# Optimization experiments

Measured on AMD Instinct MI355X. Metric: run time of the kernel, lower is better.

## Reference

```python
import jax, jax.numpy as jnp
import numpy as np

P_DROP = 0.5

def _dropout(x, key):
    keep = jax.random.bernoulli(key, 1.0 - P_DROP, x.shape)
    return jnp.where(keep, x / (1.0 - P_DROP), 0.0)

def _sage_mean_agg(src, dst, feat_src, h_self, n_dst, key):
    # SAGEMeanAgg: dropout both inputs, copy_src gather, segment mean, add, relu
    k1, k2 = jax.random.split(key)
    feat_src = _dropout(feat_src, k1)
    h_self = _dropout(h_self, k2)
    msg = feat_src[src]                                   # [E, d] gather
    summ = jax.ops.segment_sum(msg, dst, num_segments=n_dst)
    deg = jax.ops.segment_sum(jnp.ones((dst.shape[0],), msg.dtype), dst, num_segments=n_dst)
    neigh = jnp.where(deg[:, None] > 0, summ / jnp.maximum(deg, 1.0)[:, None], 0.0)
    return jax.nn.relu(neigh + h_self)

def setup_inputs() -> dict:
    key = jax.random.key(0)
    ks = jax.random.split(key, 12)
    N_total, d_in, d_hid, d_out = 1200000, 128, 256, 47
    N0, N1, N2 = 10000, 100000, 1000000
    E0, E1 = 100000, 1000000
    return {
        "features": jax.random.normal(ks[0], (N_total, d_in), jnp.float32),
        "s0": jax.random.randint(ks[1], (N0,), 0, N_total),
        "s1": jax.random.randint(ks[2], (N1,), 0, N_total),
        "s2": jax.random.randint(ks[3], (N2,), 0, N_total),
        "src0": jax.random.randint(ks[4], (E0,), 0, N1),
        "dst0": jax.random.randint(ks[5], (E0,), 0, N0),
        "src1": jax.random.randint(ks[6], (E1,), 0, N2),
        "dst1": jax.random.randint(ks[7], (E1,), 0, N1),
        "W1": jax.random.normal(ks[8], (d_in, d_hid), jnp.float32) * 0.05,
        "b1": jnp.zeros((d_hid,), jnp.float32),
        "W2": jax.random.normal(ks[9], (d_hid, d_out), jnp.float32) * 0.05,
        "b2": jnp.zeros((d_out,), jnp.float32),
    }

def reference(features, s0, s1, s2, src0, dst0, src1, dst1, W1, b1, W2, b2):
    N0, N1 = s0.shape[0], s1.shape[0]
    dk = jax.random.split(jax.random.key(42), 3)
    h0 = features[s0]
    h1 = features[s1]
    h2 = features[s2]
    # layer 0 over 2 hops (shared linear W1)
    a0 = _sage_mean_agg(src0, dst0, h1, h0, N0, dk[0])
    n0 = a0 @ W1 + b1
    a1 = _sage_mean_agg(src1, dst1, h2, h1, N1, dk[1])
    n1 = a1 @ W1 + b1
    # layer 1 over 1 hop
    a = _sage_mean_agg(src0, dst0, n1, n0, N0, dk[2])
    return a @ W2 + b2
```

## Files before the change

kernel.cpp:

```cpp
#include <hip/hip_runtime.h>
#include <hip/hip_bf16.h>

__host__ __device__ __forceinline__ unsigned rotl32(unsigned x, int d) {
  return (x << d) | (x >> (32 - d));
}

__host__ __device__ __forceinline__ void threefry2x32(
    unsigned k0, unsigned k1, unsigned x0, unsigned x1,
    unsigned& o0, unsigned& o1) {
  unsigned ks2 = k0 ^ k1 ^ 0x1BD11BDAu;
  unsigned v0 = x0 + k0, v1 = x1 + k1;
#define TF_R(r) { v0 += v1; v1 = rotl32(v1, (r)); v1 ^= v0; }
  TF_R(13) TF_R(15) TF_R(26) TF_R(6)  v0 += k1;  v1 += ks2 + 1u;
  TF_R(17) TF_R(29) TF_R(16) TF_R(24) v0 += ks2; v1 += k0 + 2u;
  TF_R(13) TF_R(15) TF_R(26) TF_R(6)  v0 += k0;  v1 += k1 + 3u;
  TF_R(17) TF_R(29) TF_R(16) TF_R(24) v0 += k1;  v1 += ks2 + 4u;
  TF_R(13) TF_R(15) TF_R(26) TF_R(6)  v0 += ks2; v1 += k0 + 5u;
#undef TF_R
  o0 = v0; o1 = v1;
}

__device__ __forceinline__ float drop_scale(unsigned ka, unsigned kb,
                                            unsigned pos) {
  unsigned o0, o1;
  threefry2x32(ka, kb, 0u, pos, o0, o1);
  return ((o0 ^ o1) >> 31) ? 0.0f : 2.0f;
}

__device__ __forceinline__ float bf2f(unsigned short u) {
  unsigned x = ((unsigned)u) << 16;
  float f;
  __builtin_memcpy(&f, &x, 4);
  return f;
}
__device__ __forceinline__ unsigned short f2bf(float f) {
  __hip_bfloat16 h = __float2bfloat16(f);
  unsigned short u;
  __builtin_memcpy(&u, &h, 2);
  return u;
}

__global__ __launch_bounds__(256) void k_count(const int* __restrict__ dst,
                                               int* __restrict__ deg, int E) {
  int e = blockIdx.x * 256 + threadIdx.x;
  if (e < E) atomicAdd(&deg[dst[e]], 1);
}

__global__ __launch_bounds__(256) void k_scan1(const int* __restrict__ d,
                                               int* __restrict__ o,
                                               int* __restrict__ bsum, int n) {
  __shared__ int ls[256];
  int t = threadIdx.x;
  int base = blockIdx.x * 1024 + t * 4;
  int v[4], s = 0;
#pragma unroll
  for (int q = 0; q < 4; ++q) {
    int i = base + q;
    v[q] = (i < n) ? d[i] : 0;
    s += v[q];
  }
  ls[t] = s;
  __syncthreads();
  for (int off = 1; off < 256; off <<= 1) {
    int x = (t >= off) ? ls[t - off] : 0;
    __syncthreads();
    ls[t] += x;
    __syncthreads();
  }
  int run = ls[t] - s;
  if (t == 255) bsum[blockIdx.x] = ls[255];
#pragma unroll
  for (int q = 0; q < 4; ++q) {
    int i = base + q;
    if (i < n) o[i] = run;
    run += v[q];
  }
}

__global__ __launch_bounds__(256) void k_scan3(int* __restrict__ o,
                                               const int* __restrict__ bx,
                                               int n) {
  int t = threadIdx.x;
  int add = bx[blockIdx.x];
  int base = blockIdx.x * 1024 + t * 4;
#pragma unroll
  for (int q = 0; q < 4; ++q) {
    int i = base + q;
    if (i < n) o[i] += add;
  }
}

__global__ __launch_bounds__(256) void k_fill(
    const int* __restrict__ src, const int* __restrict__ dst,
    const int* __restrict__ sel, const int* __restrict__ off,
    int* __restrict__ cur, int* __restrict__ csr_r, int* __restrict__ csr_g,
    int E) {
  int e = blockIdx.x * 256 + threadIdx.x;
  if (e >= E) return;
  int d = dst[e];
  int pos = off[d] + atomicAdd(&cur[d], 1);
  int r = src[e];
  csr_r[pos] = r;
  csr_g[pos] = sel[r];
}

__global__ __launch_bounds__(256) void k_agg128(
    const float* __restrict__ feats, const int* __restrict__ off,
    const int* __restrict__ csr_r, const int* __restrict__ csr_g,
    const int* __restrict__ sel_self, unsigned short* __restrict__ outbf,
    int N, unsigned kfa, unsigned kfb, unsigned kha, unsigned khb) {
  int wave = (blockIdx.x * 256 + threadIdx.x) >> 6;
  int lane = threadIdx.x & 63;
  if (wave >= N) return;
  int beg = off[wave], end = off[wave + 1];
  float acc0 = 0.f, acc1 = 0.f;
  for (int base = beg; base < end; base += 64) {
    int idx = base + lane;
    int r_l = 0, g_l = 0;
    if (idx < end) { r_l = csr_r[idx]; g_l = csr_g[idx]; }
    int cnt = min(64, end - base);
    for (int b = 0; b < cnt; ++b) {
      int r = __shfl(r_l, b), g = __shfl(g_l, b);
      float2 f = *(const float2*)(feats + (size_t)g * 128 + lane * 2);
      unsigned p = (unsigned)r * 128u + (unsigned)(lane * 2);
      acc0 += f.x * drop_scale(kfa, kfb, p);
      acc1 += f.y * drop_scale(kfa, kfb, p + 1);
    }
  }
  float deg = (float)(end - beg);
  float inv = deg > 0.f ? 1.0f / deg : 0.f;
  float n0 = acc0 * inv, n1 = acc1 * inv;
  float2 sf = *(const float2*)(feats + (size_t)sel_self[wave] * 128 + lane * 2);
  unsigned ps = (unsigned)wave * 128u + (unsigned)(lane * 2);
  float v0 = n0 + sf.x * drop_scale(kha, khb, ps);
  float v1 = n1 + sf.y * drop_scale(kha, khb, ps + 1);
  v0 = v0 > 0.f ? v0 : 0.f;
  v1 = v1 > 0.f ? v1 : 0.f;
  ushort2 u;
  u.x = f2bf(v0);
  u.y = f2bf(v1);
  *(ushort2*)(outbf + (size_t)wave * 128 + lane * 2) = u;
}

__global__ __launch_bounds__(256) void k_agg256(
    const unsigned short* __restrict__ X, const int* __restrict__ off,
    const int* __restrict__ csr_r, const unsigned short* __restrict__ self,
    unsigned short* __restrict__ outbf, int N,
    unsigned kfa, unsigned kfb, unsigned kha, unsigned khb) {
  int wave = (blockIdx.x * 256 + threadIdx.x) >> 6;
  int lane = threadIdx.x & 63;
  if (wave >= N) return;
  int beg = off[wave], end = off[wave + 1];
  float acc[4] = {0.f, 0.f, 0.f, 0.f};
  for (int base = beg; base < end; base += 64) {
    int idx = base + lane;
    int r_l = 0;
    if (idx < end) r_l = csr_r[idx];
    int cnt = min(64, end - base);
    for (int b = 0; b < cnt; ++b) {
      int r = __shfl(r_l, b);
      ushort4 raw = ((const ushort4*)(X + (size_t)r * 256))[lane];
      unsigned p = (unsigned)r * 256u + (unsigned)(lane * 4);
      acc[0] += bf2f(raw.x) * drop_scale(kfa, kfb, p);
      acc[1] += bf2f(raw.y) * drop_scale(kfa, kfb, p + 1);
      acc[2] += bf2f(raw.z) * drop_scale(kfa, kfb, p + 2);
      acc[3] += bf2f(raw.w) * drop_scale(kfa, kfb, p + 3);
    }
  }
  float deg = (float)(end - beg);
  float inv = deg > 0.f ? 1.0f / deg : 0.f;
  ushort4 sr = ((const ushort4*)(self + (size_t)wave * 256))[lane];
  unsigned ps = (unsigned)wave * 256u + (unsigned)(lane * 4);
  float sv[4] = {bf2f(sr.x), bf2f(sr.y), bf2f(sr.z), bf2f(sr.w)};
  ushort4 u;
  unsigned short* up = (unsigned short*)&u;
#pragma unroll
  for (int c = 0; c < 4; ++c) {
    float v = acc[c] * inv + sv[c] * drop_scale(kha, khb, ps + c);
    up[c] = f2bf(v > 0.f ? v : 0.f);
  }
  ((ushort4*)(outbf + (size_t)wave * 256))[lane] = u;
}

__global__ __launch_bounds__(256) void k_prepW(const float* __restrict__ W1,
                                               unsigned short* __restrict__ W1T) {
  int tid = blockIdx.x * 256 + threadIdx.x;
  int n = tid >> 7, k = tid & 127;
  W1T[n * 128 + k] = f2bf(W1[k * 256 + n]);
}

typedef short v8s __attribute__((ext_vector_type(8)));
typedef float v4f __attribute__((ext_vector_type(4)));

__global__ __launch_bounds__(256) void k_gemm1(
    const unsigned short* __restrict__ A, const unsigned short* __restrict__ W1T,
    const float* __restrict__ bias, unsigned short* __restrict__ C, int M) {
  __shared__ unsigned short As[128 * 72];
  __shared__ unsigned short Bs[128 * 72];
  const int t = threadIdx.x;
  const int r0 = blockIdx.x * 128, n0 = blockIdx.y * 128;
  const int wv = t >> 6, lane = t & 63;
  const int mb = (wv >> 1) * 64, nb = (wv & 1) * 64;
  const int qm = lane & 15, quad = lane >> 4;
  v4f acc[4][4];
#pragma unroll
  for (int i = 0; i < 4; ++i)
#pragma unroll
    for (int j = 0; j < 4; ++j) acc[i][j] = (v4f){0.f, 0.f, 0.f, 0.f};

  for (int kt = 0; kt < 128; kt += 64) {
#pragma unroll
    for (int it = 0; it < 4; ++it) {
      int i = t + it * 256;
      int r = i >> 3, c = i & 7;
      uint4 v = make_uint4(0, 0, 0, 0);
      int gr = r0 + r;
      if (gr < M) v = ((const uint4*)A)[(size_t)gr * 16 + (kt >> 3) + c];
      *(uint4*)&As[r * 72 + c * 8] = v;
    }
#pragma unroll
    for (int it = 0; it < 4; ++it) {
      int i = t + it * 256;
      int n = i >> 3, c = i & 7;
      uint4 v = ((const uint4*)W1T)[(size_t)(n0 + n) * 16 + (kt >> 3) + c];
      *(uint4*)&Bs[n * 72 + c * 8] = v;
    }
    __syncthreads();
#pragma unroll
    for (int kk = 0; kk < 64; kk += 32) {
      v8s af[4], bf_[4];
#pragma unroll
      for (int i = 0; i < 4; ++i)
        af[i] = *(const v8s*)&As[(mb + i * 16 + qm) * 72 + kk + quad * 8];
#pragma unroll
      for (int j = 0; j < 4; ++j)
        bf_[j] = *(const v8s*)&Bs[(nb + j * 16 + qm) * 72 + kk + quad * 8];
#pragma unroll
      for (int i = 0; i < 4; ++i)
#pragma unroll
        for (int j = 0; j < 4; ++j)
          acc[i][j] = __builtin_amdgcn_mfma_f32_16x16x32_bf16(
              af[i], bf_[j], acc[i][j], 0, 0, 0);
    }
    __syncthreads();
  }
  const int col_base = n0 + nb + qm;
  float bj[4];
#pragma unroll
  for (int j = 0; j < 4; ++j) bj[j] = bias[col_base + j * 16];
#pragma unroll
  for (int i = 0; i < 4; ++i) {
    int row = r0 + mb + i * 16 + quad * 4;
#pragma unroll
    for (int reg = 0; reg < 4; ++reg) {
      int rr = row + reg;
      if (rr < M) {
#pragma unroll
        for (int j = 0; j < 4; ++j)
          C[(size_t)rr * 256 + col_base + j * 16] = f2bf(acc[i][j][reg] + bj[j]);
      }
    }
  }
}

__global__ __launch_bounds__(256) void k_gemm2(
    const unsigned short* __restrict__ A, const float* __restrict__ W2,
    const float* __restrict__ b2, float* __restrict__ out, int M) {
  __shared__ float Ws[256 * 47];
  __shared__ unsigned short As[32 * 264];
  const int t = threadIdx.x;
  for (int i = t; i < 256 * 47; i += 256) Ws[i] = W2[i];
  const int r0 = blockIdx.x * 32;
#pragma unroll
  for (int it = 0; it < 4; ++it) {
    int i = t + it * 256;
    int r = i >> 5, c = i & 31;
    uint4 v = make_uint4(0, 0, 0, 0);
    if (r0 + r < M) v = ((const uint4*)A)[(size_t)(r0 + r) * 32 + c];
    *(uint4*)&As[r * 264 + c * 8] = v;
  }
  __syncthreads();
  for (int o = t; o < 32 * 47; o += 256) {
    int r = o / 47, n = o - r * 47;
    if (r0 + r >= M) continue;
    float acc = b2[n];
#pragma unroll 8
    for (int k = 0; k < 256; ++k)
      acc = fmaf(bf2f(As[r * 264 + k]), Ws[k * 47 + n], acc);
    out[(size_t)(r0 + r) * 47 + n] = acc;
  }
}

static inline size_t alignup(size_t x) { return (x + 255) & ~(size_t)255; }

extern "C" void kernel_launch(void* const* d_in, const int* in_sizes, int n_in,
                              void* d_out, int out_size, void* d_ws,
                              size_t ws_size, hipStream_t stream) {
  const float* features = (const float*)d_in[0];
  const int* s0   = (const int*)d_in[1];
  const int* s1   = (const int*)d_in[2];
  const int* s2   = (const int*)d_in[3];
  const int* src0 = (const int*)d_in[4];
  const int* dst0 = (const int*)d_in[5];
  const int* src1 = (const int*)d_in[6];
  const int* dst1 = (const int*)d_in[7];
  const float* W1 = (const float*)d_in[8];
  const float* b1 = (const float*)d_in[9];
  const float* W2 = (const float*)d_in[10];
  const float* b2 = (const float*)d_in[11];
  float* out = (float*)d_out;

  const int N0 = in_sizes[1], N1 = in_sizes[2];
  const int E0 = in_sizes[4], E1 = in_sizes[6];

  unsigned dk[3][2], kfs[3][2], khs[3][2];
  for (int i = 0; i < 3; ++i)
    threefry2x32(0u, 42u, 0u, (unsigned)i, dk[i][0], dk[i][1]);
  for (int i = 0; i < 3; ++i) {
    threefry2x32(dk[i][0], dk[i][1], 0u, 0u, kfs[i][0], kfs[i][1]);
    threefry2x32(dk[i][0], dk[i][1], 0u, 1u, khs[i][0], khs[i][1]);
  }

  char* p = (char*)d_ws;
  auto take = [&](size_t bytes) {
    char* r = p;
    p += alignup(bytes);
    return r;
  };
  unsigned short* a1bf = (unsigned short*)take((size_t)N1 * 128 * 2);
  unsigned short* n1bf = (unsigned short*)take((size_t)N1 * 256 * 2);
  unsigned short* a0bf = (unsigned short*)take((size_t)N0 * 128 * 2);
  unsigned short* n0bf = (unsigned short*)take((size_t)N0 * 256 * 2);
  unsigned short* a2bf = (unsigned short*)take((size_t)N0 * 256 * 2);
  unsigned short* w1t  = (unsigned short*)take(256 * 128 * 2);
  int* off1  = (int*)take((size_t)(N1 + 2) * 4);
  int* deg1  = (int*)take((size_t)(N1 + 2) * 4);
  int* cur1  = (int*)take((size_t)N1 * 4);
  int* off0  = (int*)take((size_t)(N0 + 2) * 4);
  int* deg0  = (int*)take((size_t)(N0 + 2) * 4);
  int* cur0  = (int*)take((size_t)N0 * 4);
  int* bsum  = (int*)take(1024 * 4);
  int* bsumx = (int*)take(1024 * 4);
  int* dummy = (int*)take(1024 * 4);
  int* csr1_r = (int*)take((size_t)E1 * 4);
  int* csr1_g = (int*)take((size_t)E1 * 4);
  int* csr0_r = (int*)take((size_t)E0 * 4);
  int* csr0_g = (int*)take((size_t)E0 * 4);

  hipMemsetAsync(deg1, 0, (size_t)(N1 + 2) * 4, stream);
  hipMemsetAsync(deg0, 0, (size_t)(N0 + 2) * 4, stream);
  hipMemsetAsync(cur1, 0, (size_t)N1 * 4, stream);
  hipMemsetAsync(cur0, 0, (size_t)N0 * 4, stream);

  k_prepW<<<128, 256, 0, stream>>>(W1, w1t);
  k_count<<<(E1 + 255) / 256, 256, 0, stream>>>(dst1, deg1, E1);
  k_count<<<(E0 + 255) / 256, 256, 0, stream>>>(dst0, deg0, E0);

  {
    int n = N1 + 1, B = (n + 1023) / 1024;
    k_scan1<<<B, 256, 0, stream>>>(deg1, off1, bsum, n);
    k_scan1<<<1, 256, 0, stream>>>(bsum, bsumx, dummy, B);
    k_scan3<<<B, 256, 0, stream>>>(off1, bsumx, n);
  }
  {
    int n = N0 + 1, B = (n + 1023) / 1024;
    k_scan1<<<B, 256, 0, stream>>>(deg0, off0, bsum, n);
    k_scan1<<<1, 256, 0, stream>>>(bsum, bsumx, dummy, B);
    k_scan3<<<B, 256, 0, stream>>>(off0, bsumx, n);
  }

  k_fill<<<(E1 + 255) / 256, 256, 0, stream>>>(src1, dst1, s2, off1, cur1,
                                               csr1_r, csr1_g, E1);
  k_fill<<<(E0 + 255) / 256, 256, 0, stream>>>(src0, dst0, s1, off0, cur0,
                                               csr0_r, csr0_g, E0);

  k_agg128<<<(N1 + 3) / 4, 256, 0, stream>>>(
      features, off1, csr1_r, csr1_g, s1, a1bf, N1,
      kfs[1][0], kfs[1][1], khs[1][0], khs[1][1]);
  {
    dim3 g((N1 + 127) / 128, 2);
    k_gemm1<<<g, 256, 0, stream>>>(a1bf, w1t, b1, n1bf, N1);
  }

  k_agg128<<<(N0 + 3) / 4, 256, 0, stream>>>(
      features, off0, csr0_r, csr0_g, s0, a0bf, N0,
      kfs[0][0], kfs[0][1], khs[0][0], khs[0][1]);
  {
    dim3 g((N0 + 127) / 128, 2);
    k_gemm1<<<g, 256, 0, stream>>>(a0bf, w1t, b1, n0bf, N0);
  }

  k_agg256<<<(N0 + 3) / 4, 256, 0, stream>>>(
      n1bf, off0, csr0_r, n0bf, a2bf, N0,
      kfs[2][0], kfs[2][1], khs[2][0], khs[2][1]);
  k_gemm2<<<(N0 + 31) / 32, 256, 0, stream>>>(a2bf, W2, b2, out, N0);
}
```

Before: 1.250 ms.

## Merge per-hop kernels into combined launches and move the second GEMM to MFMA

Graph-build, aggregation and first-GEMM kernels for both hops are merged into single launches over concatenated index ranges, which cuts the launch count. The memsets are replaced with a zero kernel. The two CSR arrays are packed into int2 and a write-offset copy replaces the separate cursor array. The 128-wide gather loop is unrolled by two. The output GEMM now uses bf16 MFMA with a hi/lo split of W2 to keep near-fp32 accuracy, in place of scalar LDS FMA; the split doubles the MFMA count.

```diff
diff --git a/kernel.cpp b/kernel.cpp
--- a/kernel.cpp
+++ b/kernel.cpp
@@ -1,5 +1,8 @@
 #include <hip/hip_runtime.h>
 #include <hip/hip_bf16.h>
+
+typedef short v8s __attribute__((ext_vector_type(8)));
+typedef float v4f __attribute__((ext_vector_type(4)));
 
 __host__ __device__ __forceinline__ unsigned rotl32(unsigned x, int d) {
   return (x << d) | (x >> (32 - d));
@@ -40,18 +43,58 @@
   return u;
 }
 
-__global__ __launch_bounds__(256) void k_count(const int* __restrict__ dst,
-                                               int* __restrict__ deg, int E) {
+__global__ __launch_bounds__(256) void k_zero(int* __restrict__ a, int na,
+                                              int* __restrict__ b, int nb) {
+  int i = blockIdx.x * 256 + threadIdx.x;
+  if (i < na) a[i] = 0;
+  if (i < nb) b[i] = 0;
+}
+
+__global__ __launch_bounds__(256) void k_prep(
+    const float* __restrict__ W1, unsigned short* __restrict__ W1T,
+    const float* __restrict__ W2, unsigned short* __restrict__ W2Th,
+    unsigned short* __restrict__ W2Tl) {
+  int tid = blockIdx.x * 256 + threadIdx.x;
+  if (tid < 32768) {
+    int n = tid >> 7, k = tid & 127;
+    W1T[n * 128 + k] = f2bf(W1[k * 256 + n]);
+  } else if (tid < 32768 + 48 * 256) {
+    int i = tid - 32768;
+    int n = i >> 8, k = i & 255;
+    float w = (n < 47) ? W2[k * 47 + n] : 0.f;
+    unsigned short hi = f2bf(w);
+    float r = w - bf2f(hi);
+    W2Th[n * 256 + k] = hi;
+    W2Tl[n * 256 + k] = f2bf(r);
+  }
+}
+
+__global__ __launch_bounds__(256) void k_countm(
+    const int* __restrict__ dst1, int* __restrict__ deg1, int E1,
+    const int* __restrict__ dst0, int* __restrict__ deg0, int E0) {
   int e = blockIdx.x * 256 + threadIdx.x;
-  if (e < E) atomicAdd(&deg[dst[e]], 1);
-}
-
-__global__ __launch_bounds__(256) void k_scan1(const int* __restrict__ d,
-                                               int* __restrict__ o,
-                                               int* __restrict__ bsum, int n) {
+  if (e < E1) {
+    atomicAdd(&deg1[dst1[e]], 1);
+  } else {
+    int e0 = e - E1;
+    if (e0 < E0) atomicAdd(&deg0[dst0[e0]], 1);
+  }
+}
+
+__global__ __launch_bounds__(256) void k_scan1m(
+    const int* __restrict__ d1, int* __restrict__ o1, int* __restrict__ b1,
+    int n1, int B1,
+    const int* __restrict__ d0, int* __restrict__ o0, int* __restrict__ b0,
+    int n0) {
   __shared__ int ls[256];
+  const int* d; int* o; int* bs; int n; int blk;
+  if ((int)blockIdx.x < B1) {
+    d = d1; o = o1; bs = b1; n = n1; blk = blockIdx.x;
+  } else {
+    d = d0; o = o0; bs = b0; n = n0; blk = blockIdx.x - B1;
+  }
   int t = threadIdx.x;
-  int base = blockIdx.x * 1024 + t * 4;
+  int base = blk * 1024 + t * 4;
   int v[4], s = 0;
 #pragma unroll
   for (int q = 0; q < 4; ++q) {
@@ -68,7 +111,7 @@
     __syncthreads();
   }
   int run = ls[t] - s;
-  if (t == 255) bsum[blockIdx.x] = ls[255];
+  if (t == 255) bs[blk] = ls[255];
 #pragma unroll
   for (int q = 0; q < 4; ++q) {
     int i = base + q;
@@ -77,49 +120,136 @@
   }
 }
 
-__global__ __launch_bounds__(256) void k_scan3(int* __restrict__ o,
-                                               const int* __restrict__ bx,
-                                               int n) {
+__device__ __forceinline__ void scan_chunk(const int* __restrict__ d,
+                                           int* __restrict__ o, int n,
+                                           int* ls) {
   int t = threadIdx.x;
-  int add = bx[blockIdx.x];
-  int base = blockIdx.x * 1024 + t * 4;
+  int base = t * 4;
+  int v[4], s = 0;
 #pragma unroll
   for (int q = 0; q < 4; ++q) {
     int i = base + q;
-    if (i < n) o[i] += add;
-  }
-}
-
-__global__ __launch_bounds__(256) void k_fill(
-    const int* __restrict__ src, const int* __restrict__ dst,
-    const int* __restrict__ sel, const int* __restrict__ off,
-    int* __restrict__ cur, int* __restrict__ csr_r, int* __restrict__ csr_g,
-    int E) {
+    v[q] = (i < n) ? d[i] : 0;
+    s += v[q];
+  }
+  ls[t] = s;
+  __syncthreads();
+  for (int off = 1; off < 256; off <<= 1) {
+    int x = (t >= off) ? ls[t - off] : 0;
+    __syncthreads();
+    ls[t] += x;
+    __syncthreads();
+  }
+  int run = ls[t] - s;
+#pragma unroll
+  for (int q = 0; q < 4; ++q) {
+    int i = base + q;
+    if (i < n) o[i] = run;
+    run += v[q];
+  }
+}
+
+__global__ __launch_bounds__(256) void k_scanmid(
+    const int* __restrict__ b1, int* __restrict__ x1, int B1,
+    const int* __restrict__ b0, int* __restrict__ x0, int B0) {
+  __shared__ int ls[256];
+  scan_chunk(b1, x1, B1, ls);
+  __syncthreads();
+  scan_chunk(b0, x0, B0, ls);
+}
+
+__global__ __launch_bounds__(256) void k_scan3m(
+    int* __restrict__ o1, int* __restrict__ w1, const int* __restrict__ x1,
+    int n1, int B1,
+    int* __restrict__ o0, int* __restrict__ w0, const int* __restrict__ x0,
+    int n0) {
+  int* o; int* w; const int* xx; int n; int blk;
+  if ((int)blockIdx.x < B1) {
+    o = o1; w = w1; xx = x1; n = n1; blk = blockIdx.x;
+  } else {
+    o = o0; w = w0; xx = x0; n = n0; blk = blockIdx.x - B1;
+  }
+  int t = threadIdx.x;
+  int add = xx[blk];
+  int base = blk * 1024 + t * 4;
+#pragma unroll
+  for (int q = 0; q < 4; ++q) {
+    int i = base + q;
+    if (i < n) {
+      int v = o[i] + add;
+      o[i] = v;
+      if (i < n - 1) w[i] = v;
+    }
+  }
+}
+
+__global__ __launch_bounds__(256) void k_fillm(
+    const int* __restrict__ src1, const int* __restrict__ dst1,
+    const int* __restrict__ s2, int* __restrict__ woff1,
+    int2* __restrict__ csr1, int E1,
+    const int* __restrict__ src0, const int* __restrict__ dst0,
+    const int* __restrict__ s1, int* __restrict__ woff0,
+    int2* __restrict__ csr0, int E0) {
   int e = blockIdx.x * 256 + threadIdx.x;
-  if (e >= E) return;
-  int d = dst[e];
-  int pos = off[d] + atomicAdd(&cur[d], 1);
-  int r = src[e];
-  csr_r[pos] = r;
-  csr_g[pos] = sel[r];
-}
-
-__global__ __launch_bounds__(256) void k_agg128(
-    const float* __restrict__ feats, const int* __restrict__ off,
-    const int* __restrict__ csr_r, const int* __restrict__ csr_g,
-    const int* __restrict__ sel_self, unsigned short* __restrict__ outbf,
-    int N, unsigned kfa, unsigned kfb, unsigned kha, unsigned khb) {
+  if (e < E1) {
+    int d = dst1[e];
+    int pos = atomicAdd(&woff1[d], 1);
+    int r = src1[e];
+    csr1[pos] = make_int2(r, s2[r]);
+  } else {
+    int e0 = e - E1;
+    if (e0 < E0) {
+      int d = dst0[e0];
+      int pos = atomicAdd(&woff0[d], 1);
+      int r = src0[e0];
+      csr0[pos] = make_int2(r, s1[r]);
+    }
+  }
+}
+
+__global__ __launch_bounds__(256) void k_agg128m(
+    const float* __restrict__ feats,
+    const int* __restrict__ off1, const int2* __restrict__ csr1,
+    const int* __restrict__ sel1,
+    const int* __restrict__ off0, const int2* __restrict__ csr0,
+    const int* __restrict__ sel0,
+    unsigned short* __restrict__ outbf, int N1, int Ntot,
+    unsigned k1fa, unsigned k1fb, unsigned k1ha, unsigned k1hb,
+    unsigned k0fa, unsigned k0fb, unsigned k0ha, unsigned k0hb) {
   int wave = (blockIdx.x * 256 + threadIdx.x) >> 6;
   int lane = threadIdx.x & 63;
-  if (wave >= N) return;
-  int beg = off[wave], end = off[wave + 1];
+  if (wave >= Ntot) return;
+  const int* off; const int2* csr; const int* sel;
+  unsigned kfa, kfb, kha, khb; int w;
+  if (wave < N1) {
+    off = off1; csr = csr1; sel = sel1;
+    kfa = k1fa; kfb = k1fb; kha = k1ha; khb = k1hb; w = wave;
+  } else {
+    off = off0; csr = csr0; sel = sel0;
+    kfa = k0fa; kfb = k0fb; kha = k0ha; khb = k0hb; w = wave - N1;
+  }
+  int beg = off[w], end = off[w + 1];
   float acc0 = 0.f, acc1 = 0.f;
   for (int base = beg; base < end; base += 64) {
     int idx = base + lane;
-    int r_l = 0, g_l = 0;
-    if (idx < end) { r_l = csr_r[idx]; g_l = csr_g[idx]; }
+    int2 rg = make_int2(0, 0);
+    if (idx < end) rg = csr[idx];
+    int r_l = rg.x, g_l = rg.y;
     int cnt = min(64, end - base);
-    for (int b = 0; b < cnt; ++b) {
+    int b = 0;
+    for (; b + 2 <= cnt; b += 2) {
+      int ra = __shfl(r_l, b),     ga = __shfl(g_l, b);
+      int rb = __shfl(r_l, b + 1), gb = __shfl(g_l, b + 1);
+      float2 fa = *(const float2*)(feats + (size_t)ga * 128 + lane * 2);
+      float2 fb = *(const float2*)(feats + (size_t)gb * 128 + lane * 2);
+      unsigned pa = (unsigned)ra * 128u + (unsigned)(lane * 2);
+      unsigned pb = (unsigned)rb * 128u + (unsigned)(lane * 2);
+      acc0 += fa.x * drop_scale(kfa, kfb, pa);
+      acc1 += fa.y * drop_scale(kfa, kfb, pa + 1);
+      acc0 += fb.x * drop_scale(kfa, kfb, pb);
+      acc1 += fb.y * drop_scale(kfa, kfb, pb + 1);
+    }
+    if (b < cnt) {
       int r = __shfl(r_l, b), g = __shfl(g_l, b);
       float2 f = *(const float2*)(feats + (size_t)g * 128 + lane * 2);
       unsigned p = (unsigned)r * 128u + (unsigned)(lane * 2);
@@ -130,8 +260,8 @@
   float deg = (float)(end - beg);
   float inv = deg > 0.f ? 1.0f / deg : 0.f;
   float n0 = acc0 * inv, n1 = acc1 * inv;
-  float2 sf = *(const float2*)(feats + (size_t)sel_self[wave] * 128 + lane * 2);
-  unsigned ps = (unsigned)wave * 128u + (unsigned)(lane * 2);
+  float2 sf = *(const float2*)(feats + (size_t)sel[w] * 128 + lane * 2);
+  unsigned ps = (unsigned)w * 128u + (unsigned)(lane * 2);
   float v0 = n0 + sf.x * drop_scale(kha, khb, ps);
   float v1 = n1 + sf.y * drop_scale(kha, khb, ps + 1);
   v0 = v0 > 0.f ? v0 : 0.f;
@@ -144,7 +274,7 @@
 
 __global__ __launch_bounds__(256) void k_agg256(
     const unsigned short* __restrict__ X, const int* __restrict__ off,
-    const int* __restrict__ csr_r, const unsigned short* __restrict__ self,
+    const int2* __restrict__ csr, const unsigned short* __restrict__ self,
     unsigned short* __restrict__ outbf, int N,
     unsigned kfa, unsigned kfb, unsigned kha, unsigned khb) {
   int wave = (blockIdx.x * 256 + threadIdx.x) >> 6;
@@ -155,7 +285,7 @@
   for (int base = beg; base < end; base += 64) {
     int idx = base + lane;
     int r_l = 0;
-    if (idx < end) r_l = csr_r[idx];
+    if (idx < end) r_l = csr[idx].x;
     int cnt = min(64, end - base);
     for (int b = 0; b < cnt; ++b) {
       int r = __shfl(r_l, b);
@@ -181,16 +311,6 @@
   }
   ((ushort4*)(outbf + (size_t)wave * 256))[lane] = u;
 }
-
-__global__ __launch_bounds__(256) void k_prepW(const float* __restrict__ W1,
-                                               unsigned short* __restrict__ W1T) {
-  int tid = blockIdx.x * 256 + threadIdx.x;
-  int n = tid >> 7, k = tid & 127;
-  W1T[n * 128 + k] = f2bf(W1[k * 256 + n]);
-}
-
-typedef short v8s __attribute__((ext_vector_type(8)));
-typedef float v4f __attribute__((ext_vector_type(4)));
 
 __global__ __launch_bounds__(256) void k_gemm1(
     const unsigned short* __restrict__ A, const unsigned short* __restrict__ W1T,
@@ -264,30 +384,40 @@
 }
 
 __global__ __launch_bounds__(256) void k_gemm2(
-    const unsigned short* __restrict__ A, const float* __restrict__ W2,
-    const float* __restrict__ b2, float* __restrict__ out, int M) {
-  __shared__ float Ws[256 * 47];
-  __shared__ unsigned short As[32 * 264];
+    const unsigned short* __restrict__ A, const unsigned short* __restrict__ Bh,
+    const unsigned short* __restrict__ Bl, const float* __restrict__ b2,
+    float* __restrict__ out, int M) {
   const int t = threadIdx.x;
-  for (int i = t; i < 256 * 47; i += 256) Ws[i] = W2[i];
-  const int r0 = blockIdx.x * 32;
-#pragma unroll
-  for (int it = 0; it < 4; ++it) {
-    int i = t + it * 256;
-    int r = i >> 5, c = i & 31;
-    uint4 v = make_uint4(0, 0, 0, 0);
-    if (r0 + r < M) v = ((const uint4*)A)[(size_t)(r0 + r) * 32 + c];
-    *(uint4*)&As[r * 264 + c * 8] = v;
-  }
-  __syncthreads();
-  for (int o = t; o < 32 * 47; o += 256) {
-    int r = o / 47, n = o - r * 47;
-    if (r0 + r >= M) continue;
-    float acc = b2[n];
-#pragma unroll 8
-    for (int k = 0; k < 256; ++k)
-      acc = fmaf(bf2f(As[r * 264 + k]), Ws[k * 47 + n], acc);
-    out[(size_t)(r0 + r) * 47 + n] = acc;
+  const int wv = t >> 6, lane = t & 63;
+  const int qm = lane & 15, quad = lane >> 4;
+  const int rw = blockIdx.x * 64 + wv * 16;
+  v4f acc[3];
+#pragma unroll
+  for (int j = 0; j < 3; ++j) acc[j] = (v4f){0.f, 0.f, 0.f, 0.f};
+  int arow = rw + qm;
+  if (arow >= M) arow = M - 1;
+  const unsigned short* Ar = A + (size_t)arow * 256;
+#pragma unroll
+  for (int kk = 0; kk < 256; kk += 32) {
+    v8s af = *(const v8s*)&Ar[kk + quad * 8];
+#pragma unroll
+    for (int j = 0; j < 3; ++j) {
+      v8s bh = *(const v8s*)&Bh[(size_t)(j * 16 + qm) * 256 + kk + quad * 8];
+      v8s bl = *(const v8s*)&Bl[(size_t)(j * 16 + qm) * 256 + kk + quad * 8];
+      acc[j] = __builtin_amdgcn_mfma_f32_16x16x32_bf16(af, bh, acc[j], 0, 0, 0);
+      acc[j] = __builtin_amdgcn_mfma_f32_16x16x32_bf16(af, bl, acc[j], 0, 0, 0);
+    }
+  }
+#pragma unroll
+  for (int j = 0; j < 3; ++j) {
+    int col = j * 16 + qm;
+    if (col >= 47) continue;
+    float bb = b2[col];
+#pragma unroll
+    for (int reg = 0; reg < 4; ++reg) {
+      int row = rw + quad * 4 + reg;
+      if (row < M) out[(size_t)row * 47 + col] = acc[j][reg] + bb;
+    }
   }
 }
 
@@ -312,6 +442,8 @@
 
   const int N0 = in_sizes[1], N1 = in_sizes[2];
   const int E0 = in_sizes[4], E1 = in_sizes[6];
+  const int Ntot = N1 + N0;
+  const int Etot = E1 + E0;
 
   unsigned dk[3][2], kfs[3][2], khs[3][2];
   for (int i = 0; i < 3; ++i)
@@ -327,71 +459,54 @@
     p += alignup(bytes);
     return r;
   };
-  unsigned short* a1bf = (unsigned short*)take((size_t)N1 * 128 * 2);
-  unsigned short* n1bf = (unsigned short*)take((size_t)N1 * 256 * 2);
-  unsigned short* a0bf = (unsigned short*)take((size_t)N0 * 128 * 2);
-  unsigned short* n0bf = (unsigned short*)take((size_t)N0 * 256 * 2);
-  unsigned short* a2bf = (unsigned short*)take((size_t)N0 * 256 * 2);
-  unsigned short* w1t  = (unsigned short*)take(256 * 128 * 2);
+  unsigned short* a_all = (unsigned short*)take((size_t)Ntot * 128 * 2);
+  unsigned short* n_all = (unsigned short*)take((size_t)Ntot * 256 * 2);
+  unsigned short* a2bf  = (unsigned short*)take((size_t)N0 * 256 * 2);
+  unsigned short* w1t   = (unsigned short*)take(256 * 128 * 2);
+  unsigned short* w2th  = (unsigned short*)take(48 * 256 * 2);
+  unsigned short* w2tl  = (unsigned short*)take(48 * 256 * 2);
   int* off1  = (int*)take((size_t)(N1 + 2) * 4);
+  int* woff1 = (int*)take((size_t)N1 * 4);
   int* deg1  = (int*)take((size_t)(N1 + 2) * 4);
-  int* cur1  = (int*)take((size_t)N1 * 4);
   int* off0  = (int*)take((size_t)(N0 + 2) * 4);
+  int* woff0 = (int*)take((size_t)N0 * 4);
   int* deg0  = (int*)take((size_t)(N0 + 2) * 4);
-  int* cur0  = (int*)take((size_t)N0 * 4);
-  int* bsum  = (int*)take(1024 * 4);
-  int* bsumx = (int*)take(1024 * 4);
-  int* dummy = (int*)take(1024 * 4);
-  int* csr1_r = (int*)take((size_t)E1 * 4);
-  int* csr1_g = (int*)take((size_t)E1 * 4);
-  int* csr0_r = (int*)take((size_t)E0 * 4);
-  int* csr0_g = (int*)take((size_t)E0 * 4);
-
-  hipMemsetAsync(deg1, 0, (size_t)(N1 + 2) * 4, stream);
-  hipMemsetAsync(deg0, 0, (size_t)(N0 + 2) * 4, stream);
-  hipMemsetAsync(cur1, 0, (size_t)N1 * 4, stream);
-  hipMemsetAsync(cur0, 0, (size_t)N0 * 4, stream);
-
-  k_prepW<<<128, 256, 0, stream>>>(W1, w1t);
-  k_count<<<(E1 + 255) / 256, 256, 0, stream>>>(dst1, deg1, E1);
-  k_count<<<(E0 + 255) / 256, 256, 0, stream>>>(dst0, deg0, E0);
-
-  {
-    int n = N1 + 1, B = (n + 1023) / 1024;
-    k_scan1<<<B, 256, 0, stream>>>(deg1, off1, bsum, n);
-    k_scan1<<<1, 256, 0, stream>>>(bsum, bsumx, dummy, B);
-    k_scan3<<<B, 256, 0, stream>>>(off1, bsumx, n);
-  }
-  {
-    int n = N0 + 1, B = (n + 1023) / 1024;
-    k_scan1<<<B, 256, 0, stream>>>(deg0, off0, bsum, n);
-    k_scan1<<<1, 256, 0, stream>>>(bsum, bsumx, dummy, B);
-    k_scan3<<<B, 256, 0, stream>>>(off0, bsumx, n);
-  }
-
-  k_fill<<<(E1 + 255) / 256, 256, 0, stream>>>(src1, dst1, s2, off1, cur1,
-                                               csr1_r, csr1_g, E1);
-  k_fill<<<(E0 + 255) / 256, 256, 0, stream>>>(src0, dst0, s1, off0, cur0,
-                                               csr0_r, csr0_g, E0);
-
-  k_agg128<<<(N1 + 3) / 4, 256, 0, stream>>>(
-      features, off1, csr1_r, csr1_g, s1, a1bf, N1,
-      kfs[1][0], kfs[1][1], khs[1][0], khs[1][1]);
-  {
-    dim3 g((N1 + 127) / 128, 2);
-    k_gemm1<<<g, 256, 0, stream>>>(a1bf, w1t, b1, n1bf, N1);
-  }
-
-  k_agg128<<<(N0 + 3) / 4, 256, 0, stream>>>(
-      features, off0, csr0_r, csr0_g, s0, a0bf, N0,
+  int* bs1   = (int*)take(1024 * 4);
+  int* bs0   = (int*)take(1024 * 4);
+  int* bx1   = (int*)take(1024 * 4);
+  int* bx0   = (int*)take(1024 * 4);
+  int2* csr1 = (int2*)take((size_t)E1 * 8);
+  int2* csr0 = (int2*)take((size_t)E0 * 8);
+
+  k_zero<<<(N1 + 2 + 255) / 256, 256, 0, stream>>>(deg1, N1 + 2, deg0, N0 + 2);
+  k_prep<<<(32768 + 48 * 256 + 255) / 256, 256, 0, stream>>>(W1, w1t, W2, w2th,
+                                                             w2tl);
+  k_countm<<<(Etot + 255) / 256, 256, 0, stream>>>(dst1, deg1, E1, dst0, deg0,
+                                                   E0);
+
+  const int n1s = N1 + 1, B1 = (n1s + 1023) / 1024;
+  const int n0s = N0 + 1, B0 = (n0s + 1023) / 1024;
+  k_scan1m<<<B1 + B0, 256, 0, stream>>>(deg1, off1, bs1, n1s, B1,
+                                        deg0, off0, bs0, n0s);
+  k_scanmid<<<1, 256, 0, stream>>>(bs1, bx1, B1, bs0, bx0, B0);
+  k_scan3m<<<B1 + B0, 256, 0, stream>>>(off1, woff1, bx1, n1s, B1,
+                                        off0, woff0, bx0, n0s);
+
+  k_fillm<<<(Etot + 255) / 256, 256, 0, stream>>>(
+      src1, dst1, s2, woff1, csr1, E1,
+      src0, dst0, s1, woff0, csr0, E0);
+
+  k_agg128m<<<(Ntot + 3) / 4, 256, 0, stream>>>(
+      features, off1, csr1, s1, off0, csr0, s0, a_all, N1, Ntot,
+      kfs[1][0], kfs[1][1], khs[1][0], khs[1][1],
       kfs[0][0], kfs[0][1], khs[0][0], khs[0][1]);
   {
-    dim3 g((N0 + 127) / 128, 2);
-    k_gemm1<<<g, 256, 0, stream>>>(a0bf, w1t, b1, n0bf, N0);
+    dim3 g((Ntot + 127) / 128, 2);
+    k_gemm1<<<g, 256, 0, stream>>>(a_all, w1t, b1, n_all, Ntot);
   }
 
   k_agg256<<<(N0 + 3) / 4, 256, 0, stream>>>(
-      n1bf, off0, csr0_r, n0bf, a2bf, N0,
+      n_all, off0, csr0, n_all + (size_t)N1 * 256, a2bf, N0,
       kfs[2][0], kfs[2][1], khs[2][0], khs[2][1]);
-  k_gemm2<<<(N0 + 31) / 32, 256, 0, stream>>>(a2bf, W2, b2, out, N0);
-}
+  k_gemm2<<<(N0 + 63) / 64, 256, 0, stream>>>(a2bf, w2th, w2tl, b2, out, N0);
+}
```

Measured after the change: 1.169 ms. -6.5%, faster.
